# Kernel optimization log

Hardware: AMD Instinct MI355X
Metric: run time of the kernel (lower is better)

Reference implementation:

```python
import jax, jax.numpy as jnp
import numpy as np

D_MODEL = 1024
N_HEADS = 16
THRESHOLD = 0.8


def setup_inputs() -> dict:
    key = jax.random.key(0)
    ks = jax.random.split(key, 12)
    B, L, D = 2, 2048, D_MODEL
    s = 1.0 / np.sqrt(D)
    return {
        "q_x": jax.random.normal(ks[0], (B, L, D), jnp.float32),
        "k_x": jax.random.normal(ks[1], (B, L, D), jnp.float32),
        "v_x": jax.random.normal(ks[2], (B, L, D), jnp.float32),
        "energy": jax.random.normal(ks[3], (B, L, D), jnp.float32),
        "Wq": jax.random.normal(ks[4], (D, D), jnp.float32) * s,
        "bq": jnp.zeros((D,), jnp.float32),
        "Wk": jax.random.normal(ks[5], (D, D), jnp.float32) * s,
        "bk": jnp.zeros((D,), jnp.float32),
        "Wv": jax.random.normal(ks[6], (D, D), jnp.float32) * s,
        "bv": jnp.zeros((D,), jnp.float32),
        "Wo": jax.random.normal(ks[7], (D, D), jnp.float32) * s,
        "bo": jnp.zeros((D,), jnp.float32),
    }


def reference(q_x, k_x, v_x, energy, Wq, bq, Wk, bk, Wv, bv, Wo, bo):
    B, L, D = q_x.shape
    H = N_HEADS
    Dh = D // H
    # projections -> (B, H, L, Dh)
    Q = (q_x @ Wq + bq).reshape(B, L, H, Dh).transpose(0, 2, 1, 3)
    K = (k_x @ Wk + bk).reshape(B, -1, H, Dh).transpose(0, 2, 1, 3)
    V = (v_x @ Wv + bv).reshape(B, -1, H, Dh).transpose(0, 2, 1, 3)
    sc = jnp.einsum("bhqd,bhkd->bhqk", Q, K) / jnp.sqrt(jnp.float32(Dh))
    # energy mask: (B, Lk) -> broadcast over heads/queries
    mask = jnp.mean(jnp.abs(energy), axis=-1) > THRESHOLD  # (B, Lk)
    sc = jnp.where(mask[:, None, None, :], sc, -jnp.inf)
    w = jnp.nan_to_num(jax.nn.softmax(sc, axis=-1), nan=0.0)
    o = jnp.einsum("bhqk,bhkd->bhqd", w, V).transpose(0, 2, 1, 3).reshape(B, L, D)
    return o @ Wo + bo
```

## Files before the change

kernel.cpp:

```cpp
#include <hip/hip_runtime.h>
#include <hip/hip_bf16.h>
#include <cstdint>

#define DEVI static __device__ __forceinline__

typedef __attribute__((ext_vector_type(8))) short s16x8;
typedef __attribute__((ext_vector_type(4))) float f32x4;
typedef __attribute__((ext_vector_type(2))) unsigned int u32x2;

DEVI unsigned short f2bf(float f) {
  union { float f; unsigned int u; } v; v.f = f;
  return (unsigned short)((v.u + 0x7FFFu + ((v.u >> 16) & 1u)) >> 16);
}

DEVI unsigned int pk2bf(float a, float b) {
  __hip_bfloat162 h2 = __float22bfloat162_rn(float2{a, b});
  return *(unsigned int*)&h2;
}

DEVI void g2l16(const void* g, void* l) {
  __builtin_amdgcn_global_load_lds((const __attribute__((address_space(1))) void*)g,
                                   (__attribute__((address_space(3))) void*)l, 16, 0, 0);
}

__global__ __launch_bounds__(256) void prep1_kernel(const float* __restrict__ q_x,
                                                    const float* __restrict__ energy,
                                                    unsigned short* __restrict__ xq,
                                                    int* __restrict__ flags,
                                                    const float* __restrict__ W0,
                                                    const float* __restrict__ W1,
                                                    const float* __restrict__ W2,
                                                    const float* __restrict__ W3,
                                                    unsigned short* __restrict__ T0,
                                                    unsigned short* __restrict__ T1,
                                                    unsigned short* __restrict__ T2,
                                                    unsigned short* __restrict__ T3) {
  const int gid = blockIdx.x;
  const int t = threadIdx.x;
  __shared__ float lds[64][65];
  if (gid < 2048) {
    int i = (gid * 256 + t) * 8;
    f32x4 x = *(const f32x4*)(q_x + i);
    f32x4 y = *(const f32x4*)(q_x + i + 4);
    s16x8 o;
    o[0] = (short)f2bf(x[0]); o[1] = (short)f2bf(x[1]);
    o[2] = (short)f2bf(x[2]); o[3] = (short)f2bf(x[3]);
    o[4] = (short)f2bf(y[0]); o[5] = (short)f2bf(y[1]);
    o[6] = (short)f2bf(y[2]); o[7] = (short)f2bf(y[3]);
    *(s16x8*)(xq + i) = o;
    return;
  }
  if (gid < 6144) {
    const int row = gid - 2048;
    f32x4 v = *(const f32x4*)(energy + (size_t)row * 1024 + t * 4);
    float s = fabsf(v[0]) + fabsf(v[1]) + fabsf(v[2]) + fabsf(v[3]);
#pragma unroll
    for (int off = 1; off < 64; off <<= 1) s += __shfl_xor(s, off);
    if ((t & 63) == 0) lds[0][t >> 6] = s;
    __syncthreads();
    if (t == 0) {
      float tot = lds[0][0] + lds[0][1] + lds[0][2] + lds[0][3];
      flags[row] = (tot * (1.0f / 1024.0f) > 0.8f) ? 1 : 0;
    }
    return;
  }
  const int x = gid - 6144;
  const int z = x >> 8, rem = x & 255;
  const float* W = z == 0 ? W0 : z == 1 ? W1 : z == 2 ? W2 : W3;
  unsigned short* WT = z == 0 ? T0 : z == 1 ? T1 : z == 2 ? T2 : T3;
  const int n0 = (rem >> 4) * 64, k0 = (rem & 15) * 64;
#pragma unroll
  for (int p = 0; p < 4; p++) {
    int r = p * 16 + (t >> 4);
    int cc = (t & 15) * 4;
    f32x4 v = *(const f32x4*)(W + (size_t)(k0 + r) * 1024 + n0 + cc);
    lds[r][cc] = v[0]; lds[r][cc + 1] = v[1]; lds[r][cc + 2] = v[2]; lds[r][cc + 3] = v[3];
  }
  __syncthreads();
  const int cc = t >> 2, gk = t & 3;
#pragma unroll
  for (int hv = 0; hv < 2; hv++) {
    s16x8 o;
#pragma unroll
    for (int j = 0; j < 8; j++) o[j] = (short)f2bf(lds[gk * 16 + hv * 8 + j][cc]);
    *(s16x8*)(WT + (size_t)(n0 + cc) * 1024 + k0 + gk * 16 + hv * 8) = o;
  }
}

__global__ __launch_bounds__(256) void scan_kernel(const int* __restrict__ flags,
                                                   int* __restrict__ inv,
                                                   int* __restrict__ cnt) {
  const int b = blockIdx.x, t = threadIdx.x;
  const int* f = flags + b * 2048;
  int* iv = inv + b * 2048;
#pragma unroll
  for (int j = 0; j < 8; j++) iv[t * 8 + j] = 0;
  int loc[8], s = 0;
#pragma unroll
  for (int j = 0; j < 8; j++) { loc[j] = f[t * 8 + j]; s += loc[j]; }
  const int lane = t & 63, w = t >> 6;
  int ps = s;
#pragma unroll
  for (int off = 1; off < 64; off <<= 1) {
    int o = __shfl_up(ps, off);
    if (lane >= off) ps += o;
  }
  __shared__ int wsum[4];
  if (lane == 63) wsum[w] = ps;
  __syncthreads();
  int woff = 0;
  for (int i = 0; i < w; i++) woff += wsum[i];
  int excl = woff + ps - s;
#pragma unroll
  for (int j = 0; j < 8; j++) {
    if (loc[j]) { iv[excl] = t * 8 + j; excl++; }
  }
  if (t == 255) cnt[b] = woff + ps;
}

__global__ __launch_bounds__(256) void prep2_kernel(const float* __restrict__ k_x,
                                                    const float* __restrict__ v_x,
                                                    const int* __restrict__ inv,
                                                    const int* __restrict__ cnt,
                                                    unsigned short* __restrict__ xkc,
                                                    unsigned short* __restrict__ xvc) {
  const int gid = blockIdx.x;
  const int t = threadIdx.x;
  const int isv = gid >> 11;
  const int lid = gid & 2047;
  const int b = lid >> 10;
  const int cp = (lid & 1023) * 2;
  const int cb = cnt[b];
  if (cp >= cb) return;
  const float* in = isv ? v_x : k_x;
  unsigned short* out = isv ? xvc : xkc;
  const int rowc = cp + (t >> 7);
  if (rowc >= cb) return;
  const int src = inv[b * 2048 + rowc];
  const int col = (t & 127) * 8;
  const float* ip = in + ((size_t)(b * 2048 + src)) * 1024 + col;
  f32x4 x = *(const f32x4*)ip;
  f32x4 y = *(const f32x4*)(ip + 4);
  s16x8 o;
  o[0] = (short)f2bf(x[0]); o[1] = (short)f2bf(x[1]);
  o[2] = (short)f2bf(x[2]); o[3] = (short)f2bf(x[3]);
  o[4] = (short)f2bf(y[0]); o[5] = (short)f2bf(y[1]);
  o[6] = (short)f2bf(y[2]); o[7] = (short)f2bf(y[3]);
  *(s16x8*)(out + ((size_t)(b * 2048 + rowc)) * 1024 + col) = o;
}

__global__ __launch_bounds__(256, 8) void proj_qkv(const unsigned short* __restrict__ xq,
                                                   const unsigned short* __restrict__ xkc,
                                                   const unsigned short* __restrict__ xvc,
                                                   const unsigned short* __restrict__ WTq,
                                                   const unsigned short* __restrict__ WTk,
                                                   const unsigned short* __restrict__ WTv,
                                                   const float* __restrict__ bq,
                                                   const float* __restrict__ bk,
                                                   const float* __restrict__ bv,
                                                   unsigned short* __restrict__ Qb,
                                                   unsigned short* __restrict__ Kc,
                                                   unsigned short* __restrict__ VTc,
                                                   const int* __restrict__ cnt,
                                                   float qsc) {
  const int z = blockIdx.z;
  const int m0 = blockIdx.x * 64;
  const int n0 = blockIdx.y * 64;
  const int b = m0 >> 11;
  const int lc0 = m0 & 2047;
  const int cb = (z == 0) ? 2048 : cnt[b];
  if (lc0 >= cb) return;

  const unsigned short* A  = z == 0 ? xq : z == 1 ? xkc : xvc;
  const unsigned short* BT = z == 0 ? WTq : z == 1 ? WTk : WTv;
  const float* bias        = z == 0 ? bq : z == 1 ? bk : bv;

  const int t = threadIdx.x;
  const int w = t >> 6, lane = t & 63;
  const int wr = w >> 1, wc = w & 1;
  const int lr = lane & 15, lg = lane >> 4;
  const int sr = lane >> 3, sg = lane & 7;

  __shared__ __align__(16) unsigned short As[64 * 64];
  __shared__ __align__(16) unsigned short Bs[64 * 64];

  f32x4 acc[2][2] = {};

  for (int kt = 0; kt < 1024; kt += 64) {
#pragma unroll
    for (int i = 0; i < 2; i++) {
      int r = (i * 4 + w) * 8 + sr;
      g2l16(A + (size_t)(m0 + r) * 1024 + kt + (sg ^ (r & 7)) * 8,
            (char*)As + (i * 4 + w) * 1024);
      g2l16(BT + (size_t)(n0 + r) * 1024 + kt + (sg ^ (r & 7)) * 8,
            (char*)Bs + (i * 4 + w) * 1024);
    }
    __syncthreads();
#pragma unroll
    for (int ks = 0; ks < 2; ks++) {
      s16x8 af[2], bf[2];
#pragma unroll
      for (int mi = 0; mi < 2; mi++) {
        int row = wr * 32 + mi * 16 + lr;
        af[mi] = *(const s16x8*)((const char*)As + row * 128 + (((ks * 4 + lg) ^ (row & 7)) * 16));
      }
#pragma unroll
      for (int nj = 0; nj < 2; nj++) {
        int row = wc * 32 + nj * 16 + lr;
        bf[nj] = *(const s16x8*)((const char*)Bs + row * 128 + (((ks * 4 + lg) ^ (row & 7)) * 16));
      }
#pragma unroll
      for (int mi = 0; mi < 2; mi++)
#pragma unroll
        for (int nj = 0; nj < 2; nj++)
          acc[mi][nj] = __builtin_amdgcn_mfma_f32_16x16x32_bf16(af[mi], bf[nj], acc[mi][nj], 0, 0, 0);
    }
    __syncthreads();
  }

  float bv2[2];
#pragma unroll
  for (int nj = 0; nj < 2; nj++) bv2[nj] = bias[n0 + wc * 32 + nj * 16 + lr];

#pragma unroll
  for (int mi = 0; mi < 2; mi++) {
    const int mloc = wr * 32 + mi * 16 + lg * 4;
#pragma unroll
    for (int nj = 0; nj < 2; nj++) {
      const int n = n0 + wc * 32 + nj * 16 + lr;
      if (z == 0) {
#pragma unroll
        for (int rg = 0; rg < 4; rg++)
          Qb[(size_t)(m0 + mloc + rg) * 1024 + n] = f2bf((acc[mi][nj][rg] + bv2[nj]) * qsc);
      } else if (z == 1) {
        const int h = n >> 6, dh = n & 63;
#pragma unroll
        for (int rg = 0; rg < 4; rg++) {
          int lc = lc0 + mloc + rg;
          if (lc < cb)
            Kc[((size_t)(b * 16 + h) * 2048 + lc) * 64 + dh] = f2bf(acc[mi][nj][rg] + bv2[nj]);
        }
      } else {
        const int h = n >> 6, dh = n & 63;
#pragma unroll
        for (int rg = 0; rg < 4; rg++) {
          int lc = lc0 + mloc + rg;
          if (lc < cb)
            VTc[((size_t)(b * 16 + h) * 64 + dh) * 2048 + lc] = f2bf(acc[mi][nj][rg] + bv2[nj]);
        }
      }
    }
  }
}

__global__ __launch_bounds__(256) void gemm_out(const unsigned short* __restrict__ A,
                                                const unsigned short* __restrict__ BT,
                                                const float* __restrict__ bias,
                                                float* __restrict__ out) {
  const int m0 = blockIdx.x * 128;
  const int n0 = blockIdx.y * 64;
  const int t = threadIdx.x;
  const int w = t >> 6, lane = t & 63;
  const int wr = w >> 1, wc = w & 1;
  const int lr = lane & 15, lg = lane >> 4;
  const int sr = lane >> 3, sg = lane & 7;

  __shared__ __align__(16) unsigned short As[128 * 64];
  __shared__ __align__(16) unsigned short Bs[64 * 64];

  f32x4 acc[4][2] = {};

  for (int kt = 0; kt < 1024; kt += 64) {
#pragma unroll
    for (int i = 0; i < 4; i++) {
      int r = (i * 4 + w) * 8 + sr;
      g2l16(A + (size_t)(m0 + r) * 1024 + kt + (sg ^ (r & 7)) * 8,
            (char*)As + (i * 4 + w) * 1024);
    }
#pragma unroll
    for (int i = 0; i < 2; i++) {
      int r = (i * 4 + w) * 8 + sr;
      g2l16(BT + (size_t)(n0 + r) * 1024 + kt + (sg ^ (r & 7)) * 8,
            (char*)Bs + (i * 4 + w) * 1024);
    }
    __syncthreads();
#pragma unroll
    for (int ks = 0; ks < 2; ks++) {
      s16x8 af[4], bf[2];
#pragma unroll
      for (int mi = 0; mi < 4; mi++) {
        int row = wr * 64 + mi * 16 + lr;
        af[mi] = *(const s16x8*)((const char*)As + row * 128 + (((ks * 4 + lg) ^ (row & 7)) * 16));
      }
#pragma unroll
      for (int nj = 0; nj < 2; nj++) {
        int row = wc * 32 + nj * 16 + lr;
        bf[nj] = *(const s16x8*)((const char*)Bs + row * 128 + (((ks * 4 + lg) ^ (row & 7)) * 16));
      }
#pragma unroll
      for (int mi = 0; mi < 4; mi++)
#pragma unroll
        for (int nj = 0; nj < 2; nj++)
          acc[mi][nj] = __builtin_amdgcn_mfma_f32_16x16x32_bf16(af[mi], bf[nj], acc[mi][nj], 0, 0, 0);
    }
    __syncthreads();
  }

  float bv2[2];
#pragma unroll
  for (int nj = 0; nj < 2; nj++) bv2[nj] = bias[n0 + wc * 32 + nj * 16 + lr];

#pragma unroll
  for (int mi = 0; mi < 4; mi++) {
    const int mb = m0 + wr * 64 + mi * 16 + lg * 4;
#pragma unroll
    for (int nj = 0; nj < 2; nj++) {
      const int n = n0 + wc * 32 + nj * 16 + lr;
#pragma unroll
      for (int rg = 0; rg < 4; rg++)
        out[(size_t)(mb + rg) * 1024 + n] = acc[mi][nj][rg] + bv2[nj];
    }
  }
}

__global__ __launch_bounds__(256) void attn_kernel(const unsigned short* __restrict__ Q,
                                                   const unsigned short* __restrict__ Kc,
                                                   const unsigned short* __restrict__ VTc,
                                                   const int* __restrict__ cnt,
                                                   unsigned short* __restrict__ O) {
  const int bh = blockIdx.x;
  const int qb = blockIdx.y;
  const int b = bh >> 4, h = bh & 15;
  const int t = threadIdx.x, w = t >> 6, lane = t & 63;
  const int lr = lane & 15, lg = lane >> 4;

  __shared__ __align__(16) unsigned short Ks[2][64 * 64];
  __shared__ __align__(16) unsigned short Vs[2][64 * 64];
  __shared__ __align__(16) unsigned short Ps[4][16 * 64];

  const size_t bh_off = (size_t)bh * 2048 * 64;
  const int q0 = qb * 64 + w * 16;
  const int cb = cnt[b];
  const int nkb = (cb + 63) >> 6;

  s16x8 qf[2];
#pragma unroll
  for (int ks = 0; ks < 2; ks++)
    qf[ks] = *(const s16x8*)(Q + ((size_t)(b * 2048 + q0 + lr)) * 1024 + h * 64 + ks * 32 + lg * 8);

  f32x4 oacc[4] = {};
  float lsum = 0.f;

  const int sr = lane >> 3, sg = lane & 7;

  auto STAGE = [&](int kb, int bb) {
#pragma unroll
    for (int i = 0; i < 2; i++) {
      int r = (i * 4 + w) * 8 + sr;
      g2l16(Kc + bh_off + (size_t)(kb * 64 + r) * 64 + (sg ^ (r & 7)) * 8,
            (char*)Ks[bb] + (i * 4 + w) * 1024);
      g2l16(VTc + bh_off + (size_t)r * 2048 + kb * 64 + (sg ^ (r & 7)) * 8,
            (char*)Vs[bb] + (i * 4 + w) * 1024);
    }
  };

  STAGE(0, 0);
  __syncthreads();
  int cur = 0;

  for (int kb = 0; kb < nkb; kb++) {
    if (kb + 1 < nkb) STAGE(kb + 1, cur ^ 1);

    float p[4][4];
    __builtin_amdgcn_s_setprio(1);
#pragma unroll
    for (int t4 = 0; t4 < 4; t4++) {
      f32x4 s = {};
#pragma unroll
      for (int ks = 0; ks < 2; ks++) {
        int row = t4 * 16 + lr;
        s16x8 kf = *(const s16x8*)((const char*)Ks[cur] + row * 128 + (((ks * 4 + lg) ^ (row & 7)) * 16));
        s = __builtin_amdgcn_mfma_f32_16x16x32_bf16(kf, qf[ks], s, 0, 0, 0);
      }
      p[t4][0] = s[0]; p[t4][1] = s[1]; p[t4][2] = s[2]; p[t4][3] = s[3];
    }
    __builtin_amdgcn_s_setprio(0);

    if ((kb + 1) * 64 <= cb) {
#pragma unroll
      for (int t4 = 0; t4 < 4; t4++)
#pragma unroll
        for (int rg = 0; rg < 4; rg++) {
          float e = __builtin_amdgcn_exp2f(p[t4][rg]);
          p[t4][rg] = e;
          lsum += e;
        }
    } else {
      const int kbase = kb * 64 + lg * 4;
#pragma unroll
      for (int t4 = 0; t4 < 4; t4++)
#pragma unroll
        for (int rg = 0; rg < 4; rg++) {
          float e = __builtin_amdgcn_exp2f(p[t4][rg]);
          e = (kbase + t4 * 16 + rg < cb) ? e : 0.f;
          p[t4][rg] = e;
          lsum += e;
        }
    }

#pragma unroll
    for (int t4 = 0; t4 < 4; t4++) {
      u32x2 pw = {pk2bf(p[t4][0], p[t4][1]), pk2bf(p[t4][2], p[t4][3])};
      int byte = lr * 128 + ((t4 * 32 + lg * 8) ^ ((lr & 7) << 4));
      *(u32x2*)((char*)Ps + w * 2048 + byte) = pw;
    }

    __builtin_amdgcn_s_setprio(1);
#pragma unroll
    for (int ks = 0; ks < 2; ks++) {
      int byteA = lr * 128 + ((ks * 64 + lg * 16) ^ ((lr & 7) << 4));
      s16x8 af = *(const s16x8*)((const char*)Ps + w * 2048 + byteA);
#pragma unroll
      for (int dt = 0; dt < 4; dt++) {
        int row = dt * 16 + lr;
        s16x8 vf = *(const s16x8*)((const char*)Vs[cur] + row * 128 + (((ks * 4 + lg) ^ (row & 7)) * 16));
        oacc[dt] = __builtin_amdgcn_mfma_f32_16x16x32_bf16(af, vf, oacc[dt], 0, 0, 0);
      }
    }
    __builtin_amdgcn_s_setprio(0);
    __syncthreads();
    cur ^= 1;
  }

  lsum += __shfl_xor(lsum, 16);
  lsum += __shfl_xor(lsum, 32);

  float rinv[4];
#pragma unroll
  for (int rg = 0; rg < 4; rg++) {
    float ls = __shfl(lsum, lg * 4 + rg);
    rinv[rg] = (ls > 0.f) ? 1.0f / ls : 0.f;
  }
#pragma unroll
  for (int dt = 0; dt < 4; dt++)
#pragma unroll
    for (int rg = 0; rg < 4; rg++) {
      int q = q0 + lg * 4 + rg;
      int d = dt * 16 + lr;
      O[((size_t)(b * 2048 + q)) * 1024 + h * 64 + d] = f2bf(oacc[dt][rg] * rinv[rg]);
    }
}

extern "C" void kernel_launch(void* const* d_in, const int* in_sizes, int n_in,
                              void* d_out, int out_size, void* d_ws, size_t ws_size,
                              hipStream_t stream) {
  (void)in_sizes; (void)n_in; (void)out_size; (void)ws_size;
  const float* q_x = (const float*)d_in[0];
  const float* k_x = (const float*)d_in[1];
  const float* v_x = (const float*)d_in[2];
  const float* energy = (const float*)d_in[3];
  const float* Wq = (const float*)d_in[4];
  const float* bq = (const float*)d_in[5];
  const float* Wk = (const float*)d_in[6];
  const float* bk = (const float*)d_in[7];
  const float* Wv = (const float*)d_in[8];
  const float* bv = (const float*)d_in[9];
  const float* Wo = (const float*)d_in[10];
  const float* bo = (const float*)d_in[11];

  char* ws = (char*)d_ws;
  const size_t MB = 1024 * 1024;
  unsigned short* xq  = (unsigned short*)(ws + 0);
  unsigned short* xkc = (unsigned short*)(ws + 8 * MB);
  unsigned short* xvc = (unsigned short*)(ws + 16 * MB);
  unsigned short* WTq = (unsigned short*)(ws + 24 * MB);
  unsigned short* WTk = (unsigned short*)(ws + 26 * MB);
  unsigned short* WTv = (unsigned short*)(ws + 28 * MB);
  unsigned short* WTo = (unsigned short*)(ws + 30 * MB);
  unsigned short* Qb  = (unsigned short*)(ws + 32 * MB);
  unsigned short* Kc  = (unsigned short*)(ws + 40 * MB);
  unsigned short* VTc = (unsigned short*)(ws + 48 * MB);
  int* flags          = (int*)(ws + 56 * MB);
  int* inv            = (int*)(ws + 56 * MB + 16 * 1024);
  int* cnt            = (int*)(ws + 56 * MB + 32 * 1024);
  unsigned short* Ob  = xq;

  const float QSC = 0.18033688011112042f;

  prep1_kernel<<<7168, 256, 0, stream>>>(q_x, energy, xq, flags,
                                         Wq, Wk, Wv, Wo, WTq, WTk, WTv, WTo);
  scan_kernel<<<2, 256, 0, stream>>>(flags, inv, cnt);
  prep2_kernel<<<4096, 256, 0, stream>>>(k_x, v_x, inv, cnt, xkc, xvc);

  proj_qkv<<<dim3(64, 16, 3), 256, 0, stream>>>(xq, xkc, xvc, WTq, WTk, WTv, bq, bk, bv,
                                                Qb, Kc, VTc, cnt, QSC);

  attn_kernel<<<dim3(32, 32), 256, 0, stream>>>(Qb, Kc, VTc, cnt, Ob);

  gemm_out<<<dim3(32, 16), 256, 0, stream>>>(Ob, WTo, bo, (float*)d_out);
}
```

Baseline: 108.4 us.

## Split attention key range across two wave groups per block with LDS merge

The attention block grows to 512 threads, and two groups of four waves each process half of the key blocks for the same 64 queries. The partial output accumulators and row sums are merged through LDS at the end. This doubles the waves working on each query tile, aiming to cut per-block latency over the sequential key loop. In exchange it drops the double-buffered prefetch: each iteration now loads and then hits a barrier before compute, so load latency is exposed, and the end-of-kernel reduction adds extra LDS traffic.

```diff
diff --git a/kernel.cpp b/kernel.cpp
--- a/kernel.cpp
+++ b/kernel.cpp
@@ -323,7 +323,7 @@
   }
 }
 
-__global__ __launch_bounds__(256) void attn_kernel(const unsigned short* __restrict__ Q,
+__global__ __launch_bounds__(512) void attn_kernel(const unsigned short* __restrict__ Q,
                                                    const unsigned short* __restrict__ Kc,
                                                    const unsigned short* __restrict__ VTc,
                                                    const int* __restrict__ cnt,
@@ -332,16 +332,18 @@
   const int qb = blockIdx.y;
   const int b = bh >> 4, h = bh & 15;
   const int t = threadIdx.x, w = t >> 6, lane = t & 63;
+  const int grp = w >> 2, wq = w & 3;
   const int lr = lane & 15, lg = lane >> 4;
 
   __shared__ __align__(16) unsigned short Ks[2][64 * 64];
   __shared__ __align__(16) unsigned short Vs[2][64 * 64];
-  __shared__ __align__(16) unsigned short Ps[4][16 * 64];
+  __shared__ __align__(16) unsigned short Ps[8][16 * 64];
 
   const size_t bh_off = (size_t)bh * 2048 * 64;
-  const int q0 = qb * 64 + w * 16;
+  const int q0 = qb * 64 + wq * 16;
   const int cb = cnt[b];
   const int nkb = (cb + 63) >> 6;
+  const int nh = (nkb + 1) >> 1;
 
   s16x8 qf[2];
 #pragma unroll
@@ -353,102 +355,106 @@
 
   const int sr = lane >> 3, sg = lane & 7;
 
-  auto STAGE = [&](int kb, int bb) {
-#pragma unroll
-    for (int i = 0; i < 2; i++) {
-      int r = (i * 4 + w) * 8 + sr;
-      g2l16(Kc + bh_off + (size_t)(kb * 64 + r) * 64 + (sg ^ (r & 7)) * 8,
-            (char*)Ks[bb] + (i * 4 + w) * 1024);
-      g2l16(VTc + bh_off + (size_t)r * 2048 + kb * 64 + (sg ^ (r & 7)) * 8,
-            (char*)Vs[bb] + (i * 4 + w) * 1024);
-    }
-  };
-
-  STAGE(0, 0);
-  __syncthreads();
-  int cur = 0;
-
-  for (int kb = 0; kb < nkb; kb++) {
-    if (kb + 1 < nkb) STAGE(kb + 1, cur ^ 1);
-
-    float p[4][4];
-    __builtin_amdgcn_s_setprio(1);
-#pragma unroll
-    for (int t4 = 0; t4 < 4; t4++) {
-      f32x4 s = {};
+  for (int i = 0; i < nh; i++) {
+    const int kb = grp ? (nh + i) : i;
+    const bool valid = (kb < nkb);
+    if (valid) {
+#pragma unroll
+      for (int ii = 0; ii < 2; ii++) {
+        int r = (ii * 4 + wq) * 8 + sr;
+        g2l16(Kc + bh_off + (size_t)(kb * 64 + r) * 64 + (sg ^ (r & 7)) * 8,
+              (char*)Ks[grp] + (ii * 4 + wq) * 1024);
+        g2l16(VTc + bh_off + (size_t)r * 2048 + kb * 64 + (sg ^ (r & 7)) * 8,
+              (char*)Vs[grp] + (ii * 4 + wq) * 1024);
+      }
+    }
+    __syncthreads();
+    if (valid) {
+      float p[4][4];
+      __builtin_amdgcn_s_setprio(1);
+#pragma unroll
+      for (int t4 = 0; t4 < 4; t4++) {
+        f32x4 s = {};
+#pragma unroll
+        for (int ks = 0; ks < 2; ks++) {
+          int row = t4 * 16 + lr;
+          s16x8 kf = *(const s16x8*)((const char*)Ks[grp] + row * 128 + (((ks * 4 + lg) ^ (row & 7)) * 16));
+          s = __builtin_amdgcn_mfma_f32_16x16x32_bf16(kf, qf[ks], s, 0, 0, 0);
+        }
+        p[t4][0] = s[0]; p[t4][1] = s[1]; p[t4][2] = s[2]; p[t4][3] = s[3];
+      }
+      __builtin_amdgcn_s_setprio(0);
+
+      if ((kb + 1) * 64 <= cb) {
+#pragma unroll
+        for (int t4 = 0; t4 < 4; t4++)
+#pragma unroll
+          for (int rg = 0; rg < 4; rg++) {
+            float e = __builtin_amdgcn_exp2f(p[t4][rg]);
+            p[t4][rg] = e;
+            lsum += e;
+          }
+      } else {
+        const int kbase = kb * 64 + lg * 4;
+#pragma unroll
+        for (int t4 = 0; t4 < 4; t4++)
+#pragma unroll
+          for (int rg = 0; rg < 4; rg++) {
+            float e = __builtin_amdgcn_exp2f(p[t4][rg]);
+            e = (kbase + t4 * 16 + rg < cb) ? e : 0.f;
+            p[t4][rg] = e;
+            lsum += e;
+          }
+      }
+
+#pragma unroll
+      for (int t4 = 0; t4 < 4; t4++) {
+        u32x2 pw = {pk2bf(p[t4][0], p[t4][1]), pk2bf(p[t4][2], p[t4][3])};
+        int byte = lr * 128 + ((t4 * 32 + lg * 8) ^ ((lr & 7) << 4));
+        *(u32x2*)((char*)Ps + w * 2048 + byte) = pw;
+      }
+
+      __builtin_amdgcn_s_setprio(1);
 #pragma unroll
       for (int ks = 0; ks < 2; ks++) {
-        int row = t4 * 16 + lr;
-        s16x8 kf = *(const s16x8*)((const char*)Ks[cur] + row * 128 + (((ks * 4 + lg) ^ (row & 7)) * 16));
-        s = __builtin_amdgcn_mfma_f32_16x16x32_bf16(kf, qf[ks], s, 0, 0, 0);
-      }
-      p[t4][0] = s[0]; p[t4][1] = s[1]; p[t4][2] = s[2]; p[t4][3] = s[3];
-    }
-    __builtin_amdgcn_s_setprio(0);
-
-    if ((kb + 1) * 64 <= cb) {
-#pragma unroll
-      for (int t4 = 0; t4 < 4; t4++)
-#pragma unroll
-        for (int rg = 0; rg < 4; rg++) {
-          float e = __builtin_amdgcn_exp2f(p[t4][rg]);
-          p[t4][rg] = e;
-          lsum += e;
+        int byteA = lr * 128 + ((ks * 64 + lg * 16) ^ ((lr & 7) << 4));
+        s16x8 af = *(const s16x8*)((const char*)Ps + w * 2048 + byteA);
+#pragma unroll
+        for (int dt = 0; dt < 4; dt++) {
+          int row = dt * 16 + lr;
+          s16x8 vf = *(const s16x8*)((const char*)Vs[grp] + row * 128 + (((ks * 4 + lg) ^ (row & 7)) * 16));
+          oacc[dt] = __builtin_amdgcn_mfma_f32_16x16x32_bf16(af, vf, oacc[dt], 0, 0, 0);
         }
-    } else {
-      const int kbase = kb * 64 + lg * 4;
-#pragma unroll
-      for (int t4 = 0; t4 < 4; t4++)
-#pragma unroll
-        for (int rg = 0; rg < 4; rg++) {
-          float e = __builtin_amdgcn_exp2f(p[t4][rg]);
-          e = (kbase + t4 * 16 + rg < cb) ? e : 0.f;
-          p[t4][rg] = e;
-          lsum += e;
-        }
-    }
-
-#pragma unroll
-    for (int t4 = 0; t4 < 4; t4++) {
-      u32x2 pw = {pk2bf(p[t4][0], p[t4][1]), pk2bf(p[t4][2], p[t4][3])};
-      int byte = lr * 128 + ((t4 * 32 + lg * 8) ^ ((lr & 7) << 4));
-      *(u32x2*)((char*)Ps + w * 2048 + byte) = pw;
-    }
-
-    __builtin_amdgcn_s_setprio(1);
-#pragma unroll
-    for (int ks = 0; ks < 2; ks++) {
-      int byteA = lr * 128 + ((ks * 64 + lg * 16) ^ ((lr & 7) << 4));
-      s16x8 af = *(const s16x8*)((const char*)Ps + w * 2048 + byteA);
-#pragma unroll
-      for (int dt = 0; dt < 4; dt++) {
-        int row = dt * 16 + lr;
-        s16x8 vf = *(const s16x8*)((const char*)Vs[cur] + row * 128 + (((ks * 4 + lg) ^ (row & 7)) * 16));
-        oacc[dt] = __builtin_amdgcn_mfma_f32_16x16x32_bf16(af, vf, oacc[dt], 0, 0, 0);
-      }
-    }
-    __builtin_amdgcn_s_setprio(0);
-    __syncthreads();
-    cur ^= 1;
+      }
+      __builtin_amdgcn_s_setprio(0);
+    }
+    __syncthreads();
   }
 
   lsum += __shfl_xor(lsum, 16);
   lsum += __shfl_xor(lsum, 32);
 
-  float rinv[4];
-#pragma unroll
-  for (int rg = 0; rg < 4; rg++) {
-    float ls = __shfl(lsum, lg * 4 + rg);
-    rinv[rg] = (ls > 0.f) ? 1.0f / ls : 0.f;
-  }
+  float* osc = grp == 0 ? (float*)Ks : (float*)Vs;
+  float* lsc = (float*)Ps;
 #pragma unroll
   for (int dt = 0; dt < 4; dt++)
 #pragma unroll
-    for (int rg = 0; rg < 4; rg++) {
-      int q = q0 + lg * 4 + rg;
-      int d = dt * 16 + lr;
-      O[((size_t)(b * 2048 + q)) * 1024 + h * 64 + d] = f2bf(oacc[dt][rg] * rinv[rg]);
-    }
+    for (int rg = 0; rg < 4; rg++)
+      osc[wq * 1024 + (lg * 4 + rg) * 64 + dt * 16 + lr] = oacc[dt][rg];
+  if (lg == 0) lsc[grp * 64 + wq * 16 + lr] = lsum;
+  __syncthreads();
+
+  if (grp == 0) {
+    const float* o0 = (const float*)Ks;
+    const float* o1 = (const float*)Vs;
+#pragma unroll
+    for (int r = 0; r < 16; r++) {
+      float l = lsc[wq * 16 + r] + lsc[64 + wq * 16 + r];
+      float rin = (l > 0.f) ? 1.0f / l : 0.f;
+      float val = (o0[wq * 1024 + r * 64 + lane] + o1[wq * 1024 + r * 64 + lane]) * rin;
+      O[((size_t)(b * 2048 + q0 + r)) * 1024 + h * 64 + lane] = f2bf(val);
+    }
+  }
 }
 
 extern "C" void kernel_launch(void* const* d_in, const int* in_sizes, int n_in,
@@ -495,7 +501,7 @@
   proj_qkv<<<dim3(64, 16, 3), 256, 0, stream>>>(xq, xkc, xvc, WTq, WTk, WTv, bq, bk, bv,
                                                 Qb, Kc, VTc, cnt, QSC);
 
-  attn_kernel<<<dim3(32, 32), 256, 0, stream>>>(Qb, Kc, VTc, cnt, Ob);
+  attn_kernel<<<dim3(32, 32), 512, 0, stream>>>(Qb, Kc, VTc, cnt, Ob);
 
   gemm_out<<<dim3(32, 16), 256, 0, stream>>>(Ob, WTo, bo, (float*)d_out);
 }
```

Measured after the change: 110.2 us. No clear change (+1.6%).
